# Optimization experiments

Hardware: AMD Instinct MI355X
Metric: run time of the kernel (lower is better)

Reference implementation:

```python
import jax, jax.numpy as jnp
import numpy as np

B, L, N, FA, FB, D, OUT, R, T = 128, 128, 6, 39, 10, 200, 1, 3, 2
MB = 256  # num bonds per molecule
NEG = -9e8


def setup_inputs():
    key = jax.random.key(0)
    ks = iter(jax.random.split(key, 64))
    def rn(shape, sc=0.05):
        return jax.random.normal(next(ks), shape, dtype=jnp.float32) * sc
    inp = {}
    inp['atom_list'] = jax.random.normal(next(ks), (B, L, FA), dtype=jnp.float32)
    inp['bond_list'] = jax.random.normal(next(ks), (B, MB, FB), dtype=jnp.float32)
    inp['atom_degree_list'] = jax.random.randint(next(ks), (B, L, N), 0, L, dtype=jnp.int32)
    inp['bond_degree_list'] = jax.random.randint(next(ks), (B, L, N), 0, MB, dtype=jnp.int32)
    inp['atom_mask'] = jnp.ones((B, L), dtype=jnp.float32)
    # parameters (torch Linear: y = x @ W + b with W stored here as [in, out])
    inp['W_atom'] = rn((FA, D)); inp['b_atom'] = rn((D,))
    inp['W_nei'] = rn((FA + FB, D)); inp['b_nei'] = rn((D,))
    inp['W_align'] = rn((R, 2 * D, 1)); inp['b_align'] = rn((R, 1))
    inp['W_attend'] = rn((R, D, D)); inp['b_attend'] = rn((R, D))
    # GRUCell weights, torch layout [3D, D], gate order r,z,n
    inp['Wih'] = rn((R, 3 * D, D)); inp['Whh'] = rn((R, 3 * D, D))
    inp['bih'] = rn((R, 3 * D)); inp['bhh'] = rn((R, 3 * D))
    inp['W_mol_align'] = rn((2 * D, 1)); inp['b_mol_align'] = rn((1,))
    inp['W_mol_attend'] = rn((D, D)); inp['b_mol_attend'] = rn((D,))
    inp['mWih'] = rn((3 * D, D)); inp['mWhh'] = rn((3 * D, D))
    inp['mbih'] = rn((3 * D,)); inp['mbhh'] = rn((3 * D,))
    inp['W_metric'] = rn((2 * D, D)); inp['b_metric'] = rn((D,))
    inp['W_out'] = rn((D, OUT)); inp['b_out'] = rn((OUT,))
    return inp


def _gather(feat, idx):
    # feat [B, M, F], idx [B, L, N] -> [B, L, N, F]
    b, l, n = idx.shape
    g = jnp.take_along_axis(feat, idx.reshape(b, l * n)[..., None], axis=1)
    return g.reshape(b, l, n, feat.shape[-1])


def _gru(x, h, Wih, Whh, bih, bhh):
    gi = x @ Wih.T + bih
    gh = h @ Whh.T + bhh
    ir, iz, inn = jnp.split(gi, 3, axis=-1)
    hr, hz, hn = jnp.split(gh, 3, axis=-1)
    r = jax.nn.sigmoid(ir + hr)
    z = jax.nn.sigmoid(iz + hz)
    n = jnp.tanh(inn + r * hn)
    return (1.0 - z) * n + z * h


def reference(atom_list, bond_list, atom_degree_list, bond_degree_list, atom_mask,
              W_atom, b_atom, W_nei, b_nei, W_align, b_align, W_attend, b_attend,
              Wih, Whh, bih, bhh, W_mol_align, b_mol_align, W_mol_attend, b_mol_attend,
              mWih, mWhh, mbih, mbhh, W_metric, b_metric, W_out, b_out):
    lrelu = jax.nn.leaky_relu
    b, l, _ = atom_list.shape
    atom_feature = lrelu(atom_list @ W_atom + b_atom)          # [B,L,D]
    atom_nei = _gather(atom_list, atom_degree_list)            # [B,L,N,FA]
    bond_nei = _gather(bond_list, bond_degree_list)            # [B,L,N,FB]
    nei = lrelu(jnp.concatenate([atom_nei, bond_nei], -1) @ W_nei + b_nei)  # [B,L,N,D]

    pad = (atom_degree_list == l - 1)
    attend_mask = (~pad).astype(jnp.float32)[..., None]        # [B,L,N,1]
    softmax_mask = jnp.where(pad, NEG, 0.0)[..., None]         # [B,L,N,1]

    h = atom_feature
    cur = atom_feature
    for r in range(R):
        if r > 0:
            nei = _gather(cur, atom_degree_list)
        exp = jnp.broadcast_to(cur[:, :, None, :], nei.shape)
        align = lrelu(jnp.concatenate([exp, nei], -1) @ W_align[r] + b_align[r])
        w = jax.nn.softmax(align + softmax_mask, axis=-2) * attend_mask
        trans = nei @ W_attend[r] + b_attend[r]
        ctx = jax.nn.elu(jnp.sum(w * trans, axis=-2))          # [B,L,D]
        h = _gru(ctx.reshape(-1, D), h.reshape(-1, D), Wih[r], Whh[r], bih[r], bhh[r]).reshape(b, l, D)
        cur = jax.nn.relu(h)

    am = atom_mask[..., None]                                   # [B,L,1]
    mol_feature = jnp.sum(cur * am, axis=-2)                    # [B,D]
    act_mol = jax.nn.relu(mol_feature)
    mol_softmax_mask = jnp.where(am == 0.0, NEG, 0.0)           # [B,L,1]
    for _ in range(T):
        exp = jnp.broadcast_to(act_mol[:, None, :], cur.shape)
        score = lrelu(jnp.concatenate([exp, cur], -1) @ W_mol_align + b_mol_align)
        w = jax.nn.softmax(score + mol_softmax_mask, axis=-2) * am
        trans = cur @ W_mol_attend + b_mol_attend
        ctx = jax.nn.elu(jnp.sum(w * trans, axis=-2))           # [B,D]
        mol_feature = _gru(ctx, mol_feature, mWih, mWhh, mbih, mbhh)
        act_mol = jax.nn.relu(mol_feature)

    dd = jnp.float32(R - 2)  # leaked python loop var `d` in the original
    feat = jnp.concatenate([mol_feature, mol_feature + dd], -1)
    return (feat @ W_metric + b_metric) @ W_out + b_out


if __name__ == '__main__':
    out = reference(**setup_inputs())
    print(out.shape)
```

## Files before the change

kernel.cpp:

```cpp
#include <hip/hip_runtime.h>
#include <hip/hip_bf16.h>
#include <math.h>
#include <string.h>

#define B_ 128
#define L_ 128
#define N_ 6
#define FA_ 39
#define FB_ 10
#define D_ 200
#define MB_ 256
#define R_ 3
#define T_ 2
#define NEGV -9e8f
#define BL_ (B_*L_)
#define G3D_ (3*D_)
#define FP32TAG 0x3F800000u
#define KP 416
#define NP 896
#define KC 224
#define NC 256

typedef __hip_bfloat16 bf16;
typedef __attribute__((ext_vector_type(8))) short short8;
typedef __attribute__((ext_vector_type(4))) float f32x4;

__device__ __forceinline__ float b2f(const bf16 x){ return __bfloat162float(x); }
__device__ __forceinline__ unsigned short f2b(float v){ bf16 t = __float2bfloat16(v); return *reinterpret_cast<unsigned short*>(&t); }
__device__ __forceinline__ float bu2f(unsigned short u){ unsigned x = ((unsigned)u)<<16; float f; memcpy(&f,&x,4); return f; }
__device__ __forceinline__ float lo2f(unsigned x){ unsigned y = x<<16; float f; memcpy(&f,&y,4); return f; }
__device__ __forceinline__ float hi2f(unsigned x){ unsigned y = x & 0xffff0000u; float f; memcpy(&f,&y,4); return f; }
__device__ __forceinline__ float lreluf(float x){ return x>=0.f ? x : 0.01f*x; }
__device__ __forceinline__ float eluf(float x){ return x>0.f ? x : expm1f(x); }
__device__ __forceinline__ float sigmf(float x){ return 1.f/(1.f+expf(-x)); }

#define NSEG 14
struct CvtArgs { const void* src[NSEG]; int ofs[NSEG+1]; };

#define PREPB_N (R_*NP*KP)
#define PREPW_N (R_*NC*KC)
#define PREPM_N (D_*G3D_)
#define PREPG_N (2*PREPM_N)
#define PREPT_N 40000
#define PREPE_N 80000
#define CONV_N 23989
#define XHPAD_N (BL_*16)
#define AROWS (BL_ + B_*MB_)
#define A_N (AROWS*64)
#define BI_N (448*64)

struct PrepArgs {
    CvtArgs cvt;
    const void *Wih, *Whh, *Watt, *mWih, *mWhh, *Wmt, *Wme;
    const void *bond, *Wnei, *atom, *Watom;
    float* conv;
    unsigned short *B2t, *WatT, *WG, *WmtT, *WmeT, *XH, *A16, *Bi16;
    const unsigned* amtag;
    int ew_total;
};

__device__ __forceinline__ float ldd(const void* p, size_t i, bool f32){
    return f32 ? ((const float*)p)[i] : b2f(((const bf16*)p)[i]);
}

__global__ void __launch_bounds__(256) k_prep(PrepArgs A){
    bool f32 = (*A.amtag == FP32TAG);
    int i = blockIdx.x*256 + (int)threadIdx.x;
    if (i >= A.ew_total) return;
    if (i < CONV_N){
        int s = 0;
        while (i >= A.cvt.ofs[s+1]) s++;
        A.conv[i] = ldd(A.cvt.src[s], i - A.cvt.ofs[s], f32);
        return;
    }
    int i2 = i - CONV_N;
    if (i2 < PREPB_N){
        int kk = i2 % KP;
        int rest = i2 / KP;
        int n = rest % NP;
        int r = rest / NP;
        float v = 0.f;
        if (kk < 200){
            if (n < 600) v = ldd(A.Wih, ((size_t)(r*G3D_ + n))*D_ + kk, f32);
        } else if (kk < 400){
            int j = -1;
            if (n < 400) j = n;
            else if (n >= 600 && n < 800) j = n - 200;
            if (j >= 0) v = ldd(A.Whh, ((size_t)(r*G3D_ + j))*D_ + (kk-200), f32);
        }
        A.B2t[i2] = f2b(v);
        return;
    }
    int i3 = i2 - PREPB_N;
    if (i3 < PREPW_N){
        int kk = i3 % KC;
        int rest = i3 / KC;
        int n = rest % NC;
        int r = rest / NC;
        float v = 0.f;
        if (kk < 200 && n < 200) v = ldd(A.Watt, ((size_t)r*D_ + kk)*D_ + n, f32);
        A.WatT[i3] = f2b(v);
        return;
    }
    int i4 = i3 - PREPW_N;
    if (i4 < PREPG_N){
        int half = i4 / PREPM_N;
        int s = i4 - half*PREPM_N;
        A.WG[(size_t)s*2 + half] = f2b(ldd(half ? A.mWhh : A.mWih, s, f32));
        return;
    }
    int i5 = i4 - PREPG_N;
    if (i5 < PREPT_N){
        int k = i5 / 200, d = i5 % 200;
        A.WmtT[(size_t)d*200 + k] = f2b(ldd(A.Wmt, i5, f32));
        return;
    }
    int i6 = i5 - PREPT_N;
    if (i6 < PREPE_N){
        int k = i6 / 200, d = i6 % 200;
        A.WmeT[(size_t)d*400 + k] = f2b(ldd(A.Wme, i6, f32));
        return;
    }
    int i7 = i6 - PREPE_N;
    if (i7 < XHPAD_N){
        int al = i7 >> 4, j = i7 & 15;
        A.XH[(size_t)al*KP + 400 + j] = 0;
        return;
    }
    int i8 = i7 - XHPAD_N;
    if (i8 < A_N){
        int row = i8 >> 6, k = i8 & 63;
        float v = 0.f;
        if (row < BL_){
            if (k < FA_) v = ldd(A.atom, (size_t)row*FA_ + k, f32);
        } else {
            int rb = row - BL_;
            if (k >= FA_ && k < FA_+FB_) v = ldd(A.bond, (size_t)rb*FB_ + (k-FA_), f32);
        }
        A.A16[i8] = f2b(v);
        return;
    }
    int i9 = i8 - A_N;
    if (i9 < BI_N){
        int n = i9 >> 6, k = i9 & 63;
        float v = 0.f;
        if (n < 200){
            if (k < FA_) v = ldd(A.Watom, (size_t)k*D_ + n, f32);
        } else if (n < 400){
            if (k < FA_+FB_) v = ldd(A.Wnei, (size_t)k*D_ + (n-200), f32);
        }
        A.Bi16[i9] = f2b(v);
    }
}

__global__ void __launch_bounds__(256) k_initmm(const unsigned short* __restrict__ A16,
        const unsigned short* __restrict__ Bi16,
        const void* __restrict__ batom, const void* __restrict__ bnei,
        unsigned short* __restrict__ XH, unsigned short* __restrict__ P16,
        unsigned short* __restrict__ Q16, const unsigned* __restrict__ amtag){
    __shared__ unsigned short As[128][40];
    __shared__ unsigned short Bs[64][40];
    bool f32 = (*amtag == FP32TAG);
    int tid = threadIdx.x;
    int mt = (int)blockIdx.x / 7, nt = (int)blockIdx.x % 7;
    int m0 = mt*128, n0 = nt*64;
    if (m0 >= BL_ && n0 + 64 <= 200) return;
    int lane = tid & 63, wv = tid >> 6;
    int quad = lane >> 4, lm = lane & 15;
    f32x4 acc[2][4];
    #pragma unroll
    for (int a=0;a<2;a++)
        #pragma unroll
        for (int b=0;b<4;b++) acc[a][b] = (f32x4){0.f,0.f,0.f,0.f};
    for (int ks = 0; ks < 2; ks++){
        int r0_ = tid >> 2, c0 = (tid & 3) * 8;
        int r1_ = (tid + 256) >> 2, c1 = ((tid + 256) & 3) * 8;
        uint4 a0 = *(const uint4*)&A16[(size_t)(m0 + r0_)*64 + ks*32 + c0];
        uint4 a1 = *(const uint4*)&A16[(size_t)(m0 + r1_)*64 + ks*32 + c1];
        uint4 b0 = *(const uint4*)&Bi16[(size_t)(n0 + (tid >> 2))*64 + ks*32 + (tid & 3)*8];
        __syncthreads();
        *(uint4*)&As[r0_][c0] = a0;
        *(uint4*)&As[r1_][c1] = a1;
        *(uint4*)&Bs[tid >> 2][(tid & 3)*8] = b0;
        __syncthreads();
        short8 av0 = *(const short8*)&As[wv*32 + lm][quad*8];
        short8 av1 = *(const short8*)&As[wv*32 + 16 + lm][quad*8];
        #pragma unroll
        for (int ns=0; ns<4; ns++){
            short8 bv = *(const short8*)&Bs[ns*16 + lm][quad*8];
            acc[0][ns] = __builtin_amdgcn_mfma_f32_16x16x32_bf16(av0, bv, acc[0][ns], 0,0,0);
            acc[1][ns] = __builtin_amdgcn_mfma_f32_16x16x32_bf16(av1, bv, acc[1][ns], 0,0,0);
        }
    }
    #pragma unroll
    for (int ms=0; ms<2; ms++)
      #pragma unroll
      for (int ns=0; ns<4; ns++){
        int n = n0 + ns*16 + lm;
        #pragma unroll
        for (int i=0;i<4;i++){
            int row = m0 + wv*32 + ms*16 + quad*4 + i;
            float v = acc[ms][ns][i];
            if (row < BL_){
                if (n < 200){
                    XH[(size_t)row*KP + 200 + n] = f2b(lreluf(v + ldd(batom, n, f32)));
                } else if (n < 400){
                    P16[(size_t)row*D_ + (n-200)] = f2b(v + ldd(bnei, n-200, f32));
                }
            } else if (n >= 200 && n < 400){
                Q16[(size_t)(row-BL_)*D_ + (n-200)] = f2b(v);
            }
        }
      }
}

__global__ void __launch_bounds__(256) k_attn(
        const unsigned short* __restrict__ cur16, const unsigned short* __restrict__ XH,
        const float* __restrict__ s1, const float* __restrict__ tb,
        const int* __restrict__ adl, const int* __restrict__ bdl,
        const unsigned short* __restrict__ P16, const unsigned short* __restrict__ Q16,
        const float* __restrict__ W_align, const float* __restrict__ b_align, int r,
        unsigned short* __restrict__ wnei, float* __restrict__ wsum){
    int bid = blockIdx.x;
    int mol = bid & (B_-1), chunk = bid >> 7;
    int wv = threadIdx.x >> 6, lane = threadIdx.x & 63;
    int al = mol*L_ + chunk*4 + wv;
    __shared__ float s_nei[4][N_][D_];

    int idxn[N_]; bool pad[N_];
    for (int n=0;n<N_;n++){ idxn[n] = adl[al*N_ + n]; pad[n] = (idxn[n] == L_-1); }

    float s2[N_];
    float s1v;
    if (r == 0){
        for (int j = lane; j < N_*D_; j += 64){
            int n = j / D_, d = j - n*D_;
            int bd = bdl[al*N_ + n];
            float acc = bu2f(P16[((size_t)mol*L_ + idxn[n])*D_ + d])
                      + bu2f(Q16[((size_t)mol*MB_ + bd)*D_ + d]);
            s_nei[wv][n][d] = lreluf(acc);
        }
        const float* Wab = W_align + D_;
        for (int n=0;n<N_;n++){
            float acc = 0.f;
            for (int d=lane; d<D_; d+=64) acc += s_nei[wv][n][d] * Wab[d];
            for (int o=32;o>0;o>>=1) acc += __shfl_xor(acc,o);
            s2[n] = acc;
        }
        float a1 = 0.f;
        for (int d=lane; d<D_; d+=64) a1 += bu2f(XH[(size_t)al*KP + 200 + d]) * W_align[d];
        for (int o=32;o>0;o>>=1) a1 += __shfl_xor(a1,o);
        s1v = a1;
    } else {
        float tmp = 0.f;
        if (lane < N_) tmp = tb[mol*L_ + idxn[lane]];
        for (int n=0;n<N_;n++) s2[n] = __shfl(tmp, n);
        s1v = s1[al];
    }

    float bav = b_align[r];
    float a[N_]; float mx = -1e30f;
    for (int n=0;n<N_;n++){
        float v = lreluf(s1v + s2[n] + bav);
        if (pad[n]) v += NEGV;
        a[n] = v; mx = fmaxf(mx, v);
    }
    float w[N_]; float se = 0.f;
    for (int n=0;n<N_;n++){ float e = expf(a[n]-mx); w[n]=e; se += e; }
    float inv = 1.f/se; float wsv = 0.f;
    for (int n=0;n<N_;n++){ w[n] = pad[n] ? 0.f : w[n]*inv; wsv += w[n]; }

    if (r == 0){
        for (int d=lane; d<D_; d+=64){
            float acc = 0.f;
            #pragma unroll
            for (int n=0;n<N_;n++) acc += w[n] * s_nei[wv][n][d];
            wnei[(size_t)al*KC + d] = f2b(acc);
        }
    } else {
        for (int d=lane; d<D_; d+=64){
            float acc = 0.f;
            #pragma unroll
            for (int n=0;n<N_;n++) acc += w[n] * bu2f(cur16[((size_t)mol*L_ + idxn[n])*KC + d]);
            wnei[(size_t)al*KC + d] = f2b(acc);
        }
    }
    if (lane < 24) wnei[(size_t)al*KC + 200 + lane] = 0;
    if (lane==0) wsum[al] = wsv;
}

__global__ void __launch_bounds__(256) k_ctxmfma(const unsigned short* __restrict__ Wn,
        const float* __restrict__ wsum, const unsigned short* __restrict__ WatT,
        const float* __restrict__ bias, int r, unsigned short* __restrict__ XH){
    __shared__ unsigned short As[128][40];
    __shared__ unsigned short Bs[64][40];
    int tid = threadIdx.x;
    int m0 = ((int)blockIdx.x & 127) * 128;
    int n0 = ((int)blockIdx.x >> 7) * 64;
    const unsigned short* Bt = WatT + (size_t)r*NC*KC;
    int lane = tid & 63, wv = tid >> 6;
    int quad = lane >> 4, lm = lane & 15;
    f32x4 acc[2][4];
    #pragma unroll
    for (int a=0;a<2;a++)
        #pragma unroll
        for (int b=0;b<4;b++) acc[a][b] = (f32x4){0.f,0.f,0.f,0.f};
    for (int ks = 0; ks < 7; ks++){
        int r0_ = tid >> 2, c0 = (tid & 3) * 8;
        int r1_ = (tid + 256) >> 2, c1 = ((tid + 256) & 3) * 8;
        uint4 a0 = *(const uint4*)&Wn[(size_t)(m0 + r0_)*KC + ks*32 + c0];
        uint4 a1 = *(const uint4*)&Wn[(size_t)(m0 + r1_)*KC + ks*32 + c1];
        uint4 b0 = *(const uint4*)&Bt[(size_t)(n0 + (tid >> 2))*KC + ks*32 + (tid & 3)*8];
        __syncthreads();
        *(uint4*)&As[r0_][c0] = a0;
        *(uint4*)&As[r1_][c1] = a1;
        *(uint4*)&Bs[tid >> 2][(tid & 3)*8] = b0;
        __syncthreads();
        short8 av0 = *(const short8*)&As[wv*32 + lm][quad*8];
        short8 av1 = *(const short8*)&As[wv*32 + 16 + lm][quad*8];
        #pragma unroll
        for (int ns=0; ns<4; ns++){
            short8 bv = *(const short8*)&Bs[ns*16 + lm][quad*8];
            acc[0][ns] = __builtin_amdgcn_mfma_f32_16x16x32_bf16(av0, bv, acc[0][ns], 0,0,0);
            acc[1][ns] = __builtin_amdgcn_mfma_f32_16x16x32_bf16(av1, bv, acc[1][ns], 0,0,0);
        }
    }
    #pragma unroll
    for (int ms=0; ms<2; ms++)
      #pragma unroll
      for (int ns=0; ns<4; ns++){
        int n = n0 + ns*16 + lm;
        if (n < 200){
            float bv = bias[r*D_ + n];
            #pragma unroll
            for (int i=0;i<4;i++){
                int row = m0 + wv*32 + ms*16 + quad*4 + i;
                float v = acc[ms][ns][i] + wsum[row]*bv;
                XH[(size_t)row*KP + n] = f2b(eluf(v));
            }
        }
      }
}

__global__ void __launch_bounds__(256) k_gemm(const unsigned short* __restrict__ XH,
        const unsigned short* __restrict__ B2t, unsigned short* __restrict__ C, int r){
    __shared__ unsigned short As[128][40];
    __shared__ unsigned short Bs[128][40];
    int tid = threadIdx.x;
    int m0 = ((int)blockIdx.x & 127) * 128;
    int n0 = ((int)blockIdx.x >> 7) * 128;
    const unsigned short* Bt = B2t + (size_t)r*NP*KP;
    int lane = tid & 63, wv = tid >> 6;
    int quad = lane >> 4, lm = lane & 15;
    f32x4 acc[2][8];
    #pragma unroll
    for (int a=0;a<2;a++)
        #pragma unroll
        for (int b=0;b<8;b++) acc[a][b] = (f32x4){0.f,0.f,0.f,0.f};
    for (int ks = 0; ks < 13; ks++){
        int r0_ = tid >> 2, c0 = (tid & 3) * 8;
        int r1_ = (tid + 256) >> 2, c1 = ((tid + 256) & 3) * 8;
        uint4 a0 = *(const uint4*)&XH[(size_t)(m0 + r0_)*KP + ks*32 + c0];
        uint4 a1 = *(const uint4*)&XH[(size_t)(m0 + r1_)*KP + ks*32 + c1];
        uint4 b0 = *(const uint4*)&Bt[(size_t)(n0 + r0_)*KP + ks*32 + c0];
        uint4 b1 = *(const uint4*)&Bt[(size_t)(n0 + r1_)*KP + ks*32 + c1];
        __syncthreads();
        *(uint4*)&As[r0_][c0] = a0;
        *(uint4*)&As[r1_][c1] = a1;
        *(uint4*)&Bs[r0_][c0] = b0;
        *(uint4*)&Bs[r1_][c1] = b1;
        __syncthreads();
        short8 av0 = *(const short8*)&As[wv*32 + lm][quad*8];
        short8 av1 = *(const short8*)&As[wv*32 + 16 + lm][quad*8];
        #pragma unroll
        for (int ns=0; ns<8; ns++){
            short8 bv = *(const short8*)&Bs[ns*16 + lm][quad*8];
            acc[0][ns] = __builtin_amdgcn_mfma_f32_16x16x32_bf16(av0, bv, acc[0][ns], 0,0,0);
            acc[1][ns] = __builtin_amdgcn_mfma_f32_16x16x32_bf16(av1, bv, acc[1][ns], 0,0,0);
        }
    }
    #pragma unroll
    for (int ms=0; ms<2; ms++)
      #pragma unroll
      for (int ns=0; ns<8; ns++)
        #pragma unroll
        for (int i=0;i<4;i++){
            int row = m0 + wv*32 + ms*16 + quad*4 + i;
            C[(size_t)row*NP + n0 + ns*16 + lm] = f2b(acc[ms][ns][i]);
        }
}

__global__ void __launch_bounds__(256) k_gru2(const unsigned short* __restrict__ C,
        unsigned short* __restrict__ XH, unsigned short* __restrict__ cur16,
        const float* __restrict__ bih, const float* __restrict__ bhh,
        const float* __restrict__ W_align, const float* __restrict__ Wma, int r,
        float* __restrict__ s1, float* __restrict__ tb, float* __restrict__ curdot){
    int wv = threadIdx.x >> 6, lane = threadIdx.x & 63;
    int al = blockIdx.x*4 + wv;
    size_t base = (size_t)al*NP;
    const float* bi = bih + r*G3D_;
    const float* bh = bhh + r*G3D_;
    const float* Wa = W_align + (r+1)*2*D_;
    bool last = (r == R_-1);
    float a1 = 0.f, a2 = 0.f;
    for (int j = lane; j < D_; j += 64){
        float rsum = bu2f(C[base + j]);
        float zsum = bu2f(C[base + 200 + j]);
        float gin  = bu2f(C[base + 400 + j]);
        float ghn  = bu2f(C[base + 600 + j]);
        float rr = sigmf(rsum + bi[j] + bh[j]);
        float zz = sigmf(zsum + bi[D_+j] + bh[D_+j]);
        float nn = tanhf(gin + bi[2*D_+j] + rr*(ghn + bh[2*D_+j]));
        size_t hx = (size_t)al*KP + 200 + j;
        float hv = bu2f(XH[hx]);
        float hn = (1.f-zz)*nn + zz*hv;
        XH[hx] = f2b(hn);
        float cv = fmaxf(hn, 0.f);
        cur16[(size_t)al*KC + j] = f2b(cv);
        if (last){
            a1 += cv * Wma[D_+j];
        } else {
            a1 += cv * Wa[j];
            a2 += cv * Wa[D_+j];
        }
    }
    if (lane < 24) cur16[(size_t)al*KC + 200 + lane] = 0;
    for (int o=32;o>0;o>>=1){ a1 += __shfl_xor(a1,o); a2 += __shfl_xor(a2,o); }
    if (lane==0){
        if (last) curdot[al] = a1;
        else { s1[al] = a1; tb[al] = a2; }
    }
}

__device__ __forceinline__ float brSum(float v, float* s_red){
    for (int o=32;o>0;o>>=1) v += __shfl_xor(v,o);
    int lane = threadIdx.x & 63, wid = threadIdx.x >> 6;
    __syncthreads();
    if (lane==0) s_red[wid] = v;
    __syncthreads();
    float r = 0.f;
    int nw = blockDim.x >> 6;
    for (int i=0;i<nw;i++) r += s_red[i];
    return r;
}

__device__ __forceinline__ float brMax(float v, float* s_red){
    for (int o=32;o>0;o>>=1) v = fmaxf(v, __shfl_xor(v,o));
    int lane = threadIdx.x & 63, wid = threadIdx.x >> 6;
    __syncthreads();
    if (lane==0) s_red[wid] = v;
    __syncthreads();
    float r = s_red[0];
    int nw = blockDim.x >> 6;
    for (int i=1;i<nw;i++) r = fmaxf(r, s_red[i]);
    return r;
}

__global__ void __launch_bounds__(512) k_mol(const unsigned short* __restrict__ cur16,
    const float* __restrict__ curdot, const float* __restrict__ atom_mask,
    const float* __restrict__ Wma, const float* __restrict__ bma,
    const unsigned short* __restrict__ WmtT, const float* __restrict__ bmt,
    const unsigned short* __restrict__ WG,
    const float* __restrict__ mbih, const float* __restrict__ mbhh,
    const unsigned short* __restrict__ WmeT, const float* __restrict__ bme,
    const float* __restrict__ Wout, const float* __restrict__ bout,
    void* __restrict__ out, const unsigned* __restrict__ amtag){
    int b = blockIdx.x, tid = threadIdx.x;
    int dq = tid & 255, cq = tid >> 8;
    __shared__ unsigned short s_cur[L_*KC];
    __shared__ float s_am[L_], s_neg[L_], s_cd[L_], s_w[L_];
    __shared__ __attribute__((aligned(16))) float s_mf[D_];
    __shared__ __attribute__((aligned(16))) float s_act[D_];
    __shared__ __attribute__((aligned(16))) float s_wc[D_];
    __shared__ __attribute__((aligned(16))) float s_ctx[D_];
    __shared__ __attribute__((aligned(16))) float s_mf2[2*D_];
    __shared__ float s_gi[G3D_], s_gh[G3D_];
    __shared__ float s_part[2][256];
    __shared__ float s_red[8];
    const uint4* src = (const uint4*)(cur16 + (size_t)b*L_*KC);
    for (int i = tid; i < L_*KC/8; i += 512) ((uint4*)s_cur)[i] = src[i];
    if (tid < L_){
        float am = atom_mask[b*L_ + tid];
        s_am[tid] = am;
        s_neg[tid] = (am == 0.f) ? NEGV : 0.f;
        s_cd[tid] = curdot[b*L_ + tid];
    }
    __syncthreads();
    {
        float a0 = 0.f, a1 = 0.f;
        if (dq < D_)
            for (int l=cq*64; l<cq*64+64; l+=2){
                a0 += bu2f(s_cur[l*KC + dq]) * s_am[l];
                a1 += bu2f(s_cur[(l+1)*KC + dq]) * s_am[l+1];
            }
        s_part[cq][dq] = a0 + a1;
        __syncthreads();
        if (tid < D_){
            float v = s_part[0][tid] + s_part[1][tid];
            s_mf[tid] = v; s_act[tid] = fmaxf(v, 0.f);
        }
        __syncthreads();
    }
    float bma0 = bma[0];
    for (int t=0;t<T_;t++){
        float p = (tid < D_) ? s_act[tid] * Wma[tid] : 0.f;
        float s1v = brSum(p, s_red);
        float sc = (tid < L_) ? (lreluf(s1v + s_cd[tid] + bma0) + s_neg[tid]) : -1e30f;
        float mx = brMax(sc, s_red);
        float e = (tid < L_) ? expf(sc - mx) : 0.f;
        float se = brSum(e, s_red);
        float wv_ = (tid < L_) ? e/se*s_am[tid] : 0.f;
        if (tid < L_) s_w[tid] = wv_;
        float wsm = brSum(wv_, s_red);
        __syncthreads();
        {
            float a0 = 0.f, a1 = 0.f;
            if (dq < D_)
                for (int l=cq*64; l<cq*64+64; l+=2){
                    a0 += s_w[l] * bu2f(s_cur[l*KC + dq]);
                    a1 += s_w[l+1] * bu2f(s_cur[(l+1)*KC + dq]);
                }
            s_part[cq][dq] = a0 + a1;
            __syncthreads();
            if (tid < D_) s_wc[tid] = s_part[0][tid] + s_part[1][tid];
            __syncthreads();
        }
        if (tid < D_){
            const uint4* wp = (const uint4*)(WmtT + (size_t)tid*200);
            float a0=0.f, a1=0.f;
            #pragma unroll 5
            for (int kk=0; kk<25; kk++){
                uint4 u = wp[kk];
                f32x4 wA = *(const f32x4*)&s_wc[8*kk];
                f32x4 wB = *(const f32x4*)&s_wc[8*kk+4];
                a0 += wA[0]*lo2f(u.x) + wA[1]*hi2f(u.x);
                a1 += wA[2]*lo2f(u.y) + wA[3]*hi2f(u.y);
                a0 += wB[0]*lo2f(u.z) + wB[1]*hi2f(u.z);
                a1 += wB[2]*lo2f(u.w) + wB[3]*hi2f(u.w);
            }
            s_ctx[tid] = eluf(a0 + a1 + wsm * bmt[tid]);
        }
        __syncthreads();
        for (int j = tid; j < G3D_; j += 512){
            const uint4* wp = (const uint4*)(WG + (size_t)j*400);
            float gi0=0.f, gi1=0.f, gh0=0.f, gh1=0.f;
            #pragma unroll 10
            for (int kk=0; kk<50; kk++){
                uint4 u = wp[kk];
                f32x4 c = *(const f32x4*)&s_ctx[4*kk];
                f32x4 m = *(const f32x4*)&s_mf[4*kk];
                gi0 += c[0]*lo2f(u.x); gh0 += m[0]*hi2f(u.x);
                gi1 += c[1]*lo2f(u.y); gh1 += m[1]*hi2f(u.y);
                gi0 += c[2]*lo2f(u.z); gh0 += m[2]*hi2f(u.z);
                gi1 += c[3]*lo2f(u.w); gh1 += m[3]*hi2f(u.w);
            }
            s_gi[j] = gi0+gi1; s_gh[j] = gh0+gh1;
        }
        __syncthreads();
        if (tid < D_){
            int d = tid;
            float rr = sigmf(s_gi[d] + mbih[d] + s_gh[d] + mbhh[d]);
            float zz = sigmf(s_gi[D_+d] + mbih[D_+d] + s_gh[D_+d] + mbhh[D_+d]);
            float nn = tanhf(s_gi[2*D_+d] + mbih[2*D_+d] + rr*(s_gh[2*D_+d] + mbhh[2*D_+d]));
            float nm = (1.f-zz)*nn + zz*s_mf[d];
            s_mf[d] = nm; s_act[d] = fmaxf(nm, 0.f);
        }
        __syncthreads();
    }
    const float dd = (float)(R_ - 2);
    if (tid < 2*D_) s_mf2[tid] = (tid < D_) ? s_mf[tid] : s_mf[tid - D_] + dd;
    __syncthreads();
    float p2 = 0.f;
    if (tid < D_){
        const uint4* wp = (const uint4*)(WmeT + (size_t)tid*400);
        float a0=0.f, a1=0.f;
        #pragma unroll 10
        for (int kk=0; kk<50; kk++){
            uint4 u = wp[kk];
            f32x4 wA = *(const f32x4*)&s_mf2[8*kk];
            f32x4 wB = *(const f32x4*)&s_mf2[8*kk+4];
            a0 += wA[0]*lo2f(u.x) + wA[1]*hi2f(u.x);
            a1 += wA[2]*lo2f(u.y) + wA[3]*hi2f(u.y);
            a0 += wB[0]*lo2f(u.z) + wB[1]*hi2f(u.z);
            a1 += wB[2]*lo2f(u.w) + wB[3]*hi2f(u.w);
        }
        p2 = (a0 + a1 + bme[tid]) * Wout[tid];
    }
    float o = brSum(p2, s_red);
    if (tid==0){
        o += bout[0];
        if (*amtag == FP32TAG) ((float*)out)[b] = o;
        else ((bf16*)out)[b] = __float2bfloat16(o);
    }
}

extern "C" void kernel_launch(void* const* d_in, const int* in_sizes, int n_in,
                              void* d_out, int out_size, void* d_ws, size_t ws_size,
                              hipStream_t stream) {
    const int* adl = (const int*)d_in[2];
    const int* bdl = (const int*)d_in[3];
    const unsigned* amtag = (const unsigned*)d_in[4];

    static const int srcidx[NSEG] = {4,9,10,12,15,16,17,18,20,23,24,26,27,28};
    static const int segsz[NSEG]  = {16384,1200,3,600,1800,1800,400,1,200,600,600,200,200,1};
    CvtArgs ca;
    int ofs[NSEG+1]; ofs[0] = 0;
    for (int i=0;i<NSEG;i++){ ca.src[i] = d_in[srcidx[i]]; ca.ofs[i] = ofs[i]; ofs[i+1] = ofs[i] + segsz[i]; }
    ca.ofs[NSEG] = ofs[NSEG];

    float* ws   = (float*)d_ws;
    float* conv = ws;
    unsigned short* XH    = (unsigned short*)(conv + 24000);
    unsigned short* B2t   = XH + (size_t)BL_*KP;
    unsigned short* WatT  = B2t + PREPB_N;
    unsigned short* WG    = WatT + PREPW_N;
    unsigned short* WmtT  = WG + PREPG_N;
    unsigned short* WmeT  = WmtT + PREPT_N;
    unsigned short* Bi16  = WmeT + PREPE_N;
    unsigned short* cur16 = Bi16 + BI_N;
    unsigned short* creg  = cur16 + (size_t)BL_*KC;
    unsigned short* C = creg;
    unsigned short* A16  = creg;
    unsigned short* wnei = creg;
    unsigned short* Q16  = creg + (size_t)BL_*KC;
    unsigned short* P16  = Q16 + (size_t)B_*MB_*D_;
    float* s1     = (float*)(creg + (size_t)BL_*NP);
    float* tb     = s1 + BL_;
    float* wsum   = tb + BL_;
    float* curdot = wsum + BL_;

    const float* c_amask = conv + ofs[0];
    const float* c_Walign= conv + ofs[1];
    const float* c_balign= conv + ofs[2];
    const float* c_batt  = conv + ofs[3];
    const float* c_bih   = conv + ofs[4];
    const float* c_bhh   = conv + ofs[5];
    const float* c_Wma   = conv + ofs[6];
    const float* c_bma   = conv + ofs[7];
    const float* c_bmt   = conv + ofs[8];
    const float* c_mbih  = conv + ofs[9];
    const float* c_mbhh  = conv + ofs[10];
    const float* c_bme   = conv + ofs[11];
    const float* c_Wout  = conv + ofs[12];
    const float* c_bout  = conv + ofs[13];

    PrepArgs A;
    A.cvt = ca;
    A.Wih = d_in[13]; A.Whh = d_in[14]; A.Watt = d_in[11];
    A.mWih = d_in[21]; A.mWhh = d_in[22]; A.Wmt = d_in[19]; A.Wme = d_in[25];
    A.bond = d_in[1]; A.Wnei = d_in[7]; A.atom = d_in[0]; A.Watom = d_in[5];
    A.conv = conv;
    A.B2t = B2t; A.WatT = WatT; A.WG = WG; A.WmtT = WmtT; A.WmeT = WmeT;
    A.XH = XH; A.A16 = A16; A.Bi16 = Bi16;
    A.amtag = amtag;
    A.ew_total = CONV_N + PREPB_N + PREPW_N + PREPG_N + PREPT_N + PREPE_N
               + XHPAD_N + A_N + BI_N;

    k_prep<<<(A.ew_total + 255)/256, 256, 0, stream>>>(A);
    k_initmm<<<(AROWS/128)*7, 256, 0, stream>>>(A16, Bi16, d_in[6], d_in[8],
                                                XH, P16, Q16, amtag);

    for (int r=0; r<R_; r++){
        k_attn<<<BL_/4, 256, 0, stream>>>(cur16, XH, s1, tb, adl, bdl, P16, Q16,
                                          c_Walign, c_balign, r, wnei, wsum);
        k_ctxmfma<<<(BL_/128)*(NC/64), 256, 0, stream>>>(wnei, wsum, WatT, c_batt, r, XH);
        k_gemm<<<(BL_/128)*(NP/128), 256, 0, stream>>>(XH, B2t, C, r);
        k_gru2<<<BL_/4, 256, 0, stream>>>(C, XH, cur16, c_bih, c_bhh,
                                          c_Walign, c_Wma, r, s1, tb, curdot);
    }

    k_mol<<<B_, 512, 0, stream>>>(cur16, curdot, c_amask, c_Wma, c_bma, WmtT, c_bmt,
                                  WG, c_mbih, c_mbhh, WmeT, c_bme, c_Wout, c_bout,
                                  d_out, amtag);
}
```

Before: 439.4 us.

## Overlap mol GRU hidden-gate matvec with attention softmax across wave groups

The interleaved mol GRU weight buffer is split into separate input and hidden matrices. Waves 0-3 of k_mol now compute the attention softmax with wave-local shuffles, dropping the block-wide reductions and their barriers, and then the weighted context sum. Waves 4-7 compute the hidden-state gate matvec in parallel, since it depends only on the previous mol_feature. Biases are cached in shared memory and dot loops are fully unrolled. The redundant per-wave softmax and the single-thread 128-length context loop may add latency, and k_mol is only a small part of total runtime.

```diff
diff --git a/kernel.cpp b/kernel.cpp
--- a/kernel.cpp
+++ b/kernel.cpp
@@ -54,7 +54,7 @@
     const void *Wih, *Whh, *Watt, *mWih, *mWhh, *Wmt, *Wme;
     const void *bond, *Wnei, *atom, *Watom;
     float* conv;
-    unsigned short *B2t, *WatT, *WG, *WmtT, *WmeT, *XH, *A16, *Bi16;
+    unsigned short *B2t, *WatT, *WGi, *WGh, *WmtT, *WmeT, *XH, *A16, *Bi16;
     const unsigned* amtag;
     int ew_total;
 };
@@ -106,7 +106,7 @@
     if (i4 < PREPG_N){
         int half = i4 / PREPM_N;
         int s = i4 - half*PREPM_N;
-        A.WG[(size_t)s*2 + half] = f2b(ldd(half ? A.mWhh : A.mWih, s, f32));
+        (half ? A.WGh : A.WGi)[s] = f2b(ldd(half ? A.mWhh : A.mWih, s, f32));
         return;
     }
     int i5 = i4 - PREPG_N;
@@ -444,39 +444,48 @@
     return r;
 }
 
-__device__ __forceinline__ float brMax(float v, float* s_red){
-    for (int o=32;o>0;o>>=1) v = fmaxf(v, __shfl_xor(v,o));
-    int lane = threadIdx.x & 63, wid = threadIdx.x >> 6;
-    __syncthreads();
-    if (lane==0) s_red[wid] = v;
-    __syncthreads();
-    float r = s_red[0];
-    int nw = blockDim.x >> 6;
-    for (int i=1;i<nw;i++) r = fmaxf(r, s_red[i]);
-    return r;
+__device__ __forceinline__ float dot200(const unsigned short* __restrict__ wrow,
+                                        const float* __restrict__ v){
+    const uint4* wp = (const uint4*)wrow;
+    float a0=0.f, a1=0.f;
+    #pragma unroll
+    for (int kk=0; kk<25; kk++){
+        uint4 u = wp[kk];
+        f32x4 A = *(const f32x4*)&v[8*kk];
+        f32x4 Bv = *(const f32x4*)&v[8*kk+4];
+        a0 += A[0]*lo2f(u.x) + A[1]*hi2f(u.x);
+        a1 += A[2]*lo2f(u.y) + A[3]*hi2f(u.y);
+        a0 += Bv[0]*lo2f(u.z) + Bv[1]*hi2f(u.z);
+        a1 += Bv[2]*lo2f(u.w) + Bv[3]*hi2f(u.w);
+    }
+    return a0 + a1;
 }
 
 __global__ void __launch_bounds__(512) k_mol(const unsigned short* __restrict__ cur16,
     const float* __restrict__ curdot, const float* __restrict__ atom_mask,
     const float* __restrict__ Wma, const float* __restrict__ bma,
     const unsigned short* __restrict__ WmtT, const float* __restrict__ bmt,
-    const unsigned short* __restrict__ WG,
+    const unsigned short* __restrict__ WGi, const unsigned short* __restrict__ WGh,
     const float* __restrict__ mbih, const float* __restrict__ mbhh,
     const unsigned short* __restrict__ WmeT, const float* __restrict__ bme,
     const float* __restrict__ Wout, const float* __restrict__ bout,
     void* __restrict__ out, const unsigned* __restrict__ amtag){
     int b = blockIdx.x, tid = threadIdx.x;
+    int wv = tid >> 6, lane = tid & 63;
     int dq = tid & 255, cq = tid >> 8;
     __shared__ unsigned short s_cur[L_*KC];
-    __shared__ float s_am[L_], s_neg[L_], s_cd[L_], s_w[L_];
+    __shared__ float s_am[L_], s_neg[L_], s_cd[L_];
+    __shared__ float s_wp[4][L_];
     __shared__ __attribute__((aligned(16))) float s_mf[D_];
     __shared__ __attribute__((aligned(16))) float s_act[D_];
     __shared__ __attribute__((aligned(16))) float s_wc[D_];
     __shared__ __attribute__((aligned(16))) float s_ctx[D_];
     __shared__ __attribute__((aligned(16))) float s_mf2[2*D_];
     __shared__ float s_gi[G3D_], s_gh[G3D_];
+    __shared__ float s_wma[D_], s_bmt[D_], s_bi[G3D_], s_bh[G3D_];
     __shared__ float s_part[2][256];
     __shared__ float s_red[8];
+    __shared__ float s_wsm;
     const uint4* src = (const uint4*)(cur16 + (size_t)b*L_*KC);
     for (int i = tid; i < L_*KC/8; i += 512) ((uint4*)s_cur)[i] = src[i];
     if (tid < L_){
@@ -484,6 +493,11 @@
         s_am[tid] = am;
         s_neg[tid] = (am == 0.f) ? NEGV : 0.f;
         s_cd[tid] = curdot[b*L_ + tid];
+    }
+    if (tid < D_){ s_wma[tid] = Wma[tid]; s_bmt[tid] = bmt[tid]; }
+    for (int j = tid; j < G3D_; j += 512){
+        s_bi[j] = mbih[j];
+        s_bh[j] = mbhh[j];
     }
     __syncthreads();
     {
@@ -503,65 +517,59 @@
     }
     float bma0 = bma[0];
     for (int t=0;t<T_;t++){
-        float p = (tid < D_) ? s_act[tid] * Wma[tid] : 0.f;
-        float s1v = brSum(p, s_red);
-        float sc = (tid < L_) ? (lreluf(s1v + s_cd[tid] + bma0) + s_neg[tid]) : -1e30f;
-        float mx = brMax(sc, s_red);
-        float e = (tid < L_) ? expf(sc - mx) : 0.f;
-        float se = brSum(e, s_red);
-        float wv_ = (tid < L_) ? e/se*s_am[tid] : 0.f;
-        if (tid < L_) s_w[tid] = wv_;
-        float wsm = brSum(wv_, s_red);
+        if (wv < 4){
+            float a = s_act[lane]*s_wma[lane] + s_act[lane+64]*s_wma[lane+64];
+            a += s_act[lane+128]*s_wma[lane+128];
+            if (lane < 8) a += s_act[lane+192]*s_wma[lane+192];
+            #pragma unroll
+            for (int o=32;o>0;o>>=1) a += __shfl_xor(a,o);
+            float sc0 = lreluf(a + s_cd[lane] + bma0) + s_neg[lane];
+            float sc1 = lreluf(a + s_cd[lane+64] + bma0) + s_neg[lane+64];
+            float m = fmaxf(sc0, sc1);
+            #pragma unroll
+            for (int o=32;o>0;o>>=1) m = fmaxf(m, __shfl_xor(m,o));
+            float e0 = expf(sc0 - m), e1 = expf(sc1 - m);
+            float s = e0 + e1;
+            #pragma unroll
+            for (int o=32;o>0;o>>=1) s += __shfl_xor(s,o);
+            float inv = 1.f/s;
+            float w0 = e0*inv*s_am[lane], w1 = e1*inv*s_am[lane+64];
+            float ws = w0 + w1;
+            #pragma unroll
+            for (int o=32;o>0;o>>=1) ws += __shfl_xor(ws,o);
+            s_wp[wv][lane] = w0; s_wp[wv][lane+64] = w1;
+            if (tid == 0) s_wsm = ws;
+            if (tid < D_){
+                float acc = 0.f;
+                #pragma unroll 16
+                for (int l=0; l<L_; l++)
+                    acc += s_wp[wv][l] * bu2f(s_cur[l*KC + tid]);
+                s_wc[tid] = acc;
+            }
+        } else {
+            int h = tid - 256;
+            s_gh[h]       = dot200(WGh + (size_t)h*D_,       s_mf);
+            s_gh[h+256]   = dot200(WGh + (size_t)(h+256)*D_, s_mf);
+            if (h < 88)
+                s_gh[h+512] = dot200(WGh + (size_t)(h+512)*D_, s_mf);
+        }
+        __syncthreads();
+        if (tid < D_){
+            float acc = dot200(WmtT + (size_t)tid*D_, s_wc);
+            s_ctx[tid] = eluf(acc + s_wsm * s_bmt[tid]);
+        }
         __syncthreads();
         {
-            float a0 = 0.f, a1 = 0.f;
-            if (dq < D_)
-                for (int l=cq*64; l<cq*64+64; l+=2){
-                    a0 += s_w[l] * bu2f(s_cur[l*KC + dq]);
-                    a1 += s_w[l+1] * bu2f(s_cur[(l+1)*KC + dq]);
-                }
-            s_part[cq][dq] = a0 + a1;
-            __syncthreads();
-            if (tid < D_) s_wc[tid] = s_part[0][tid] + s_part[1][tid];
-            __syncthreads();
-        }
-        if (tid < D_){
-            const uint4* wp = (const uint4*)(WmtT + (size_t)tid*200);
-            float a0=0.f, a1=0.f;
-            #pragma unroll 5
-            for (int kk=0; kk<25; kk++){
-                uint4 u = wp[kk];
-                f32x4 wA = *(const f32x4*)&s_wc[8*kk];
-                f32x4 wB = *(const f32x4*)&s_wc[8*kk+4];
-                a0 += wA[0]*lo2f(u.x) + wA[1]*hi2f(u.x);
-                a1 += wA[2]*lo2f(u.y) + wA[3]*hi2f(u.y);
-                a0 += wB[0]*lo2f(u.z) + wB[1]*hi2f(u.z);
-                a1 += wB[2]*lo2f(u.w) + wB[3]*hi2f(u.w);
-            }
-            s_ctx[tid] = eluf(a0 + a1 + wsm * bmt[tid]);
-        }
-        __syncthreads();
-        for (int j = tid; j < G3D_; j += 512){
-            const uint4* wp = (const uint4*)(WG + (size_t)j*400);
-            float gi0=0.f, gi1=0.f, gh0=0.f, gh1=0.f;
-            #pragma unroll 10
-            for (int kk=0; kk<50; kk++){
-                uint4 u = wp[kk];
-                f32x4 c = *(const f32x4*)&s_ctx[4*kk];
-                f32x4 m = *(const f32x4*)&s_mf[4*kk];
-                gi0 += c[0]*lo2f(u.x); gh0 += m[0]*hi2f(u.x);
-                gi1 += c[1]*lo2f(u.y); gh1 += m[1]*hi2f(u.y);
-                gi0 += c[2]*lo2f(u.z); gh0 += m[2]*hi2f(u.z);
-                gi1 += c[3]*lo2f(u.w); gh1 += m[3]*hi2f(u.w);
-            }
-            s_gi[j] = gi0+gi1; s_gh[j] = gh0+gh1;
+            s_gi[tid] = dot200(WGi + (size_t)tid*D_, s_ctx);
+            if (tid < 88)
+                s_gi[tid+512] = dot200(WGi + (size_t)(tid+512)*D_, s_ctx);
         }
         __syncthreads();
         if (tid < D_){
             int d = tid;
-            float rr = sigmf(s_gi[d] + mbih[d] + s_gh[d] + mbhh[d]);
-            float zz = sigmf(s_gi[D_+d] + mbih[D_+d] + s_gh[D_+d] + mbhh[D_+d]);
-            float nn = tanhf(s_gi[2*D_+d] + mbih[2*D_+d] + rr*(s_gh[2*D_+d] + mbhh[2*D_+d]));
+            float rr = sigmf(s_gi[d] + s_bi[d] + s_gh[d] + s_bh[d]);
+            float zz = sigmf(s_gi[D_+d] + s_bi[D_+d] + s_gh[D_+d] + s_bh[D_+d]);
+            float nn = tanhf(s_gi[2*D_+d] + s_bi[2*D_+d] + rr*(s_gh[2*D_+d] + s_bh[2*D_+d]));
             float nm = (1.f-zz)*nn + zz*s_mf[d];
             s_mf[d] = nm; s_act[d] = fmaxf(nm, 0.f);
         }
@@ -574,7 +582,7 @@
     if (tid < D_){
         const uint4* wp = (const uint4*)(WmeT + (size_t)tid*400);
         float a0=0.f, a1=0.f;
-        #pragma unroll 10
+        #pragma unroll
         for (int kk=0; kk<50; kk++){
             uint4 u = wp[kk];
             f32x4 wA = *(const f32x4*)&s_mf2[8*kk];
@@ -613,8 +621,9 @@
     unsigned short* XH    = (unsigned short*)(conv + 24000);
     unsigned short* B2t   = XH + (size_t)BL_*KP;
     unsigned short* WatT  = B2t + PREPB_N;
-    unsigned short* WG    = WatT + PREPW_N;
-    unsigned short* WmtT  = WG + PREPG_N;
+    unsigned short* WGi   = WatT + PREPW_N;
+    unsigned short* WGh   = WGi + PREPM_N;
+    unsigned short* WmtT  = WGh + PREPM_N;
     unsigned short* WmeT  = WmtT + PREPT_N;
     unsigned short* Bi16  = WmeT + PREPE_N;
     unsigned short* cur16 = Bi16 + BI_N;
@@ -650,7 +659,7 @@
     A.mWih = d_in[21]; A.mWhh = d_in[22]; A.Wmt = d_in[19]; A.Wme = d_in[25];
     A.bond = d_in[1]; A.Wnei = d_in[7]; A.atom = d_in[0]; A.Watom = d_in[5];
     A.conv = conv;
-    A.B2t = B2t; A.WatT = WatT; A.WG = WG; A.WmtT = WmtT; A.WmeT = WmeT;
+    A.B2t = B2t; A.WatT = WatT; A.WGi = WGi; A.WGh = WGh; A.WmtT = WmtT; A.WmeT = WmeT;
     A.XH = XH; A.A16 = A16; A.Bi16 = Bi16;
     A.amtag = amtag;
     A.ew_total = CONV_N + PREPB_N + PREPW_N + PREPG_N + PREPT_N + PREPE_N
@@ -670,6 +679,6 @@
     }
 
     k_mol<<<B_, 512, 0, stream>>>(cur16, curdot, c_amask, c_Wma, c_bma, WmtT, c_bmt,
-                                  WG, c_mbih, c_mbhh, WmeT, c_bme, c_Wout, c_bout,
+                                  WGi, WGh, c_mbih, c_mbhh, WmeT, c_bme, c_Wout, c_bout,
                                   d_out, amtag);
 }
```

After: 484.7 us. 1.1x slower.
